# Kernel tuning notes

Hardware: AMD Instinct MI355X
Metric: run time of the kernel (lower is better)

Reference implementation:

```python
import jax, jax.numpy as jnp
import numpy as np

ENTREG = 0.1          # blur passed to geomloss SamplesLoss
P_EXP = 2             # p=2 -> squared euclidean cost
EPS = ENTREG ** P_EXP # geomloss temperature eps = blur**p = 0.01
N_ITERS = 30          # fixed Sinkhorn iterations (geomloss tensorized loop)


def _squared_distances(x, y):
    # C[i,j] = ||x_i - y_j||^2  (geomloss.utils.squared_distances)
    x2 = jnp.sum(x * x, axis=-1)  # [n]
    y2 = jnp.sum(y * y, axis=-1)  # [m]
    return x2[:, None] + y2[None, :] - 2.0 * (x @ y.T)


def setup_inputs() -> dict:
    key = jax.random.key(0)
    k1, k2 = jax.random.split(key)
    Xs = jax.random.normal(k1, (4096, 1024), dtype=jnp.float32)
    Xt = jax.random.normal(k2, (4096, 1024), dtype=jnp.float32)
    return {"Xs": Xs, "Xt": Xt}


def _sinkhorn_plan(Xs, Xt):
    n, m = Xs.shape[0], Xt.shape[0]
    C = _squared_distances(Xs, Xt)          # [n, m]
    loga = -jnp.log(jnp.float32(n))         # uniform source weights (log)
    logb = -jnp.log(jnp.float32(m))         # uniform target weights (log)
    f0 = jnp.zeros((n,), dtype=C.dtype)
    g0 = jnp.zeros((m,), dtype=C.dtype)

    def step(carry, _):
        f, g = carry
        # softmin updates in log-domain (stable logsumexp), eps = blur**p
        g = -EPS * jax.nn.logsumexp((f[:, None] - C) / EPS + loga, axis=0)  # [m]
        f = -EPS * jax.nn.logsumexp((g[None, :] - C) / EPS + logb, axis=1)  # [n]
        return (f, g), None

    (f, g), _ = jax.lax.scan(jax.checkpoint(step), (f0, g0), None, length=N_ITERS)
    # closs: P = exp((u^T + v - C) / entreg)  -- note: entreg, not eps, as in source
    P = jnp.exp((f[:, None] + g[None, :] - C) / ENTREG)
    return P


def reference(Xs, Xt):
    return _sinkhorn_plan(Xs, Xt)
```

## Files before the change

kernel.cpp:

```cpp
#include <hip/hip_runtime.h>
#include <cstddef>
#include <cstdint>

#define N_PTS 4096
#define DIMK 1024

typedef _Float16 half8 __attribute__((ext_vector_type(8)));
typedef float floatx4 __attribute__((ext_vector_type(4)));

static constexpr float S_SCALE = 144.26950408889634f;
static constexpr float TWO_S   = 288.53900817779268f;
static constexpr float NEG_BIG = -3.4e38f;


__global__ __launch_bounds__(256) void k_prep(const float* __restrict__ Xs,
                                              float* __restrict__ fvec) {
  int row  = blockIdx.x * 4 + (threadIdx.x >> 6);
  int lane = threadIdx.x & 63;
  const float* src = Xs + (size_t)row * DIMK;
  float s = 0.f;
#pragma unroll
  for (int r = 0; r < 4; ++r) {
    float4 a = *(const float4*)(src + lane * 4 + r * 256);
    s += a.x * a.x + a.y * a.y + a.z * a.z + a.w * a.w;
  }
#pragma unroll
  for (int off = 32; off; off >>= 1) s += __shfl_xor(s, off);
  if (lane == 0) fvec[row] = (1024.0f - s) * S_SCALE;
}

__global__ __launch_bounds__(256) void k_convert(const float* __restrict__ X,
                                                 _Float16* __restrict__ H,
                                                 _Float16* __restrict__ L) {
  size_t i8 = ((size_t)blockIdx.x * 256 + threadIdx.x) * 8;
  float4 a = *(const float4*)(X + i8);
  float4 b = *(const float4*)(X + i8 + 4);
  float v[8] = {a.x, a.y, a.z, a.w, b.x, b.y, b.z, b.w};
  half8 h, l;
#pragma unroll
  for (int q = 0; q < 8; ++q) {
    _Float16 hh = (_Float16)v[q];
    h[q] = hh;
    l[q] = (_Float16)(v[q] - (float)hh);
  }
  *(half8*)(H + i8) = h;
  *(half8*)(L + i8) = l;
}

__global__ __launch_bounds__(256) void k_gemm_mfma(const _Float16* __restrict__ Ah,
                                                   const _Float16* __restrict__ Al,
                                                   const _Float16* __restrict__ Bh,
                                                   const _Float16* __restrict__ Bl,
                                                   float* __restrict__ D,
                                                   float* __restrict__ DT) {
  __shared__ __align__(16) _Float16 Ahs[128 * 32];
  __shared__ __align__(16) _Float16 Als[128 * 32];
  __shared__ __align__(16) _Float16 Bhs[128 * 32];
  __shared__ __align__(16) _Float16 Bls[128 * 32];
  const int t    = threadIdx.x;
  const int lane = t & 63, wave = t >> 6;
  const int wm = wave >> 1, wn = wave & 1;
  const int lm = lane & 15, q = lane >> 4;
  const int row0 = blockIdx.y * 128, col0 = blockIdx.x * 128;

  floatx4 acc[4][4];
#pragma unroll
  for (int i = 0; i < 4; ++i)
#pragma unroll
    for (int j = 0; j < 4; ++j) acc[i][j] = (floatx4){0.f, 0.f, 0.f, 0.f};

  const int r0 = t >> 2, p0 = t & 3;
  const int r1 = 64 + r0;

  for (int k0 = 0; k0 < DIMK; k0 += 32) {
    size_t ga0 = (size_t)(row0 + r0) * DIMK + k0 + p0 * 8;
    size_t ga1 = (size_t)(row0 + r1) * DIMK + k0 + p0 * 8;
    size_t gb0 = (size_t)(col0 + r0) * DIMK + k0 + p0 * 8;
    size_t gb1 = (size_t)(col0 + r1) * DIMK + k0 + p0 * 8;
    half8 vah0 = *(const half8*)(Ah + ga0);
    half8 vah1 = *(const half8*)(Ah + ga1);
    half8 val0 = *(const half8*)(Al + ga0);
    half8 val1 = *(const half8*)(Al + ga1);
    half8 vbh0 = *(const half8*)(Bh + gb0);
    half8 vbh1 = *(const half8*)(Bh + gb1);
    half8 vbl0 = *(const half8*)(Bl + gb0);
    half8 vbl1 = *(const half8*)(Bl + gb1);
    __syncthreads();
    ((half8*)Ahs)[t] = vah0; ((half8*)Ahs)[t + 256] = vah1;
    ((half8*)Als)[t] = val0; ((half8*)Als)[t + 256] = val1;
    ((half8*)Bhs)[t] = vbh0; ((half8*)Bhs)[t + 256] = vbh1;
    ((half8*)Bls)[t] = vbl0; ((half8*)Bls)[t + 256] = vbl1;
    __syncthreads();

    half8 afh[4], afl[4], bfh[4], bfl[4];
#pragma unroll
    for (int i = 0; i < 4; ++i) {
      int ar = (wm * 64 + i * 16 + lm) * 32 + q * 8;
      int br = (wn * 64 + i * 16 + lm) * 32 + q * 8;
      afh[i] = *(const half8*)(Ahs + ar);
      afl[i] = *(const half8*)(Als + ar);
      bfh[i] = *(const half8*)(Bhs + br);
      bfl[i] = *(const half8*)(Bls + br);
    }
#pragma unroll
    for (int i = 0; i < 4; ++i)
#pragma unroll
      for (int j = 0; j < 4; ++j) {
        acc[i][j] = __builtin_amdgcn_mfma_f32_16x16x32_f16(afh[i], bfh[j], acc[i][j], 0, 0, 0);
        acc[i][j] = __builtin_amdgcn_mfma_f32_16x16x32_f16(afh[i], bfl[j], acc[i][j], 0, 0, 0);
        acc[i][j] = __builtin_amdgcn_mfma_f32_16x16x32_f16(afl[i], bfh[j], acc[i][j], 0, 0, 0);
      }
  }

#pragma unroll
  for (int i = 0; i < 4; ++i) {
    int mbase = row0 + wm * 64 + i * 16 + q * 4;
#pragma unroll
    for (int j = 0; j < 4; ++j) {
      int n = col0 + wn * 64 + j * 16 + lm;
      float vals[4];
#pragma unroll
      for (int r = 0; r < 4; ++r) {
        float vv = -TWO_S * acc[i][j][r];
        vals[r] = vv;
        D[(size_t)(mbase + r) * N_PTS + n] = vv;
      }
      if (DT) *(float4*)(DT + (size_t)n * N_PTS + mbase) = *(float4*)vals;
    }
  }
}

__global__ __launch_bounds__(256) void k_gemm(const float* __restrict__ A,
                                              const float* __restrict__ B,
                                              float* __restrict__ D) {
  __shared__ float As[16][132];
  __shared__ float Bs[16][132];
  const int t  = threadIdx.x;
  const int tx = t & 15, ty = t >> 4;
  const int row0 = blockIdx.y * 128, col0 = blockIdx.x * 128;
  float acc[8][8];
#pragma unroll
  for (int i = 0; i < 8; ++i)
#pragma unroll
    for (int j = 0; j < 8; ++j) acc[i][j] = 0.f;
  for (int k0 = 0; k0 < DIMK; k0 += 16) {
#pragma unroll
    for (int s2 = 0; s2 < 2; ++s2) {
      int f4i = t + s2 * 256;
      int r   = f4i >> 2;
      int kp  = (f4i & 3) << 2;
      float4 a4 = *(const float4*)(A + (size_t)(row0 + r) * DIMK + k0 + kp);
      float4 b4 = *(const float4*)(B + (size_t)(col0 + r) * DIMK + k0 + kp);
      As[kp + 0][r] = a4.x; As[kp + 1][r] = a4.y; As[kp + 2][r] = a4.z; As[kp + 3][r] = a4.w;
      Bs[kp + 0][r] = b4.x; Bs[kp + 1][r] = b4.y; Bs[kp + 2][r] = b4.z; Bs[kp + 3][r] = b4.w;
    }
    __syncthreads();
#pragma unroll
    for (int kk = 0; kk < 16; ++kk) {
      float a[8], b[8];
      *(float4*)(a)     = *(const float4*)(&As[kk][ty * 4]);
      *(float4*)(a + 4) = *(const float4*)(&As[kk][64 + ty * 4]);
      *(float4*)(b)     = *(const float4*)(&Bs[kk][tx * 4]);
      *(float4*)(b + 4) = *(const float4*)(&Bs[kk][64 + tx * 4]);
#pragma unroll
      for (int i = 0; i < 8; ++i)
#pragma unroll
        for (int j = 0; j < 8; ++j) acc[i][j] = fmaf(a[i], b[j], acc[i][j]);
    }
    __syncthreads();
  }
#pragma unroll
  for (int i = 0; i < 8; ++i) {
    int r = row0 + ((i < 4) ? (ty * 4 + i) : (64 + ty * 4 + (i - 4)));
    float* out = D + (size_t)r * N_PTS + col0;
    float4 o1, o2;
    o1.x = -TWO_S * acc[i][0]; o1.y = -TWO_S * acc[i][1];
    o1.z = -TWO_S * acc[i][2]; o1.w = -TWO_S * acc[i][3];
    o2.x = -TWO_S * acc[i][4]; o2.y = -TWO_S * acc[i][5];
    o2.z = -TWO_S * acc[i][6]; o2.w = -TWO_S * acc[i][7];
    *(float4*)(out + tx * 4)      = o1;
    *(float4*)(out + 64 + tx * 4) = o2;
  }
}

__global__ __launch_bounds__(256) void k_sweep(const float* __restrict__ Mrow,
                                               const float* __restrict__ vin,
                                               float* __restrict__ vout) {
  const int t = threadIdx.x;
  const int l = t & 63;
  const int row = blockIdx.x * 4 + (t >> 6);
  const float* rp_ = Mrow + (size_t)row * N_PTS;
  float M = NEG_BIG, S = 0.f;
#pragma unroll
  for (int c = 0; c < 4; ++c) {
    float v[16];
#pragma unroll
    for (int qq = 0; qq < 4; ++qq) {
      int j = l * 4 + (c * 4 + qq) * 256;
      float4 d = *(const float4*)(rp_ + j);
      float4 g = *(const float4*)(vin + j);
      v[qq * 4 + 0] = g.x - d.x;
      v[qq * 4 + 1] = g.y - d.y;
      v[qq * 4 + 2] = g.z - d.z;
      v[qq * 4 + 3] = g.w - d.w;
    }
    float Mc = v[0];
#pragma unroll
    for (int qq = 1; qq < 16; ++qq) Mc = fmaxf(Mc, v[qq]);
    float Mn = fmaxf(M, Mc);
    float s  = S * exp2f(M - Mn);
#pragma unroll
    for (int qq = 0; qq < 16; ++qq) s += exp2f(v[qq] - Mn);
    M = Mn; S = s;
  }
#pragma unroll
  for (int off = 32; off; off >>= 1) {
    float M2 = __shfl_xor(M, off);
    float S2 = __shfl_xor(S, off);
    float Mn = fmaxf(M, M2);
    S = S * exp2f(M - Mn) + S2 * exp2f(M2 - Mn);
    M = Mn;
  }
  if (l == 0) vout[row] = 12.0f - M - log2f(S);
}

__device__ __forceinline__ float4 f4max(float4 a, float4 b) {
  return make_float4(fmaxf(a.x, b.x), fmaxf(a.y, b.y), fmaxf(a.z, b.z), fmaxf(a.w, b.w));
}
__device__ __forceinline__ void msmerge(float4& M, float4& S, const float4 M2, const float4 S2) {
  float4 Mn = f4max(M, M2);
  S.x = S.x * exp2f(M.x - Mn.x) + S2.x * exp2f(M2.x - Mn.x);
  S.y = S.y * exp2f(M.y - Mn.y) + S2.y * exp2f(M2.y - Mn.y);
  S.z = S.z * exp2f(M.z - Mn.z) + S2.z * exp2f(M2.z - Mn.z);
  S.w = S.w * exp2f(M.w - Mn.w) + S2.w * exp2f(M2.w - Mn.w);
  M = Mn;
}
__global__ __launch_bounds__(1024) void k_colpass(const float* __restrict__ D,
                                                  const float* __restrict__ fvec,
                                                  float* __restrict__ gvec) {
  __shared__ float fs[N_PTS];
  __shared__ float4 MS[16][4][2];
  const int t = threadIdx.x;
  *(float4*)(fs + t * 4) = *(const float4*)(fvec + t * 4);
  __syncthreads();
  const int c4 = t & 3;
  const int rp = t >> 2;
  const float* base = D + blockIdx.x * 16 + c4 * 4;
  float4 M = make_float4(NEG_BIG, NEG_BIG, NEG_BIG, NEG_BIG);
  float4 S = make_float4(0.f, 0.f, 0.f, 0.f);
#pragma unroll
  for (int h = 0; h < 2; ++h) {
    float4 v[8];
#pragma unroll
    for (int qq = 0; qq < 8; ++qq) {
      int r = rp + (h * 8 + qq) * 256;
      float4 d = *(const float4*)(base + (size_t)r * N_PTS);
      float fr = fs[r];
      v[qq] = make_float4(fr - d.x, fr - d.y, fr - d.z, fr - d.w);
    }
    float4 Mc = f4max(f4max(f4max(v[0], v[1]), f4max(v[2], v[3])),
                      f4max(f4max(v[4], v[5]), f4max(v[6], v[7])));
    float4 Mn = f4max(M, Mc);
    float4 s;
    s.x = S.x * exp2f(M.x - Mn.x);
    s.y = S.y * exp2f(M.y - Mn.y);
    s.z = S.z * exp2f(M.z - Mn.z);
    s.w = S.w * exp2f(M.w - Mn.w);
#pragma unroll
    for (int qq = 0; qq < 8; ++qq) {
      s.x += exp2f(v[qq].x - Mn.x);
      s.y += exp2f(v[qq].y - Mn.y);
      s.z += exp2f(v[qq].z - Mn.z);
      s.w += exp2f(v[qq].w - Mn.w);
    }
    M = Mn; S = s;
  }
#pragma unroll
  for (int off = 4; off <= 32; off <<= 1) {
    float4 M2, S2;
    M2.x = __shfl_xor(M.x, off); M2.y = __shfl_xor(M.y, off);
    M2.z = __shfl_xor(M.z, off); M2.w = __shfl_xor(M.w, off);
    S2.x = __shfl_xor(S.x, off); S2.y = __shfl_xor(S.y, off);
    S2.z = __shfl_xor(S.z, off); S2.w = __shfl_xor(S.w, off);
    msmerge(M, S, M2, S2);
  }
  const int wv = t >> 6, l = t & 63;
  if (l < 4) { MS[wv][l][0] = M; MS[wv][l][1] = S; }
  __syncthreads();
  if (t < 4) {
    float4 M0 = MS[0][t][0], S0 = MS[0][t][1];
#pragma unroll
    for (int w = 1; w < 16; ++w) msmerge(M0, S0, MS[w][t][0], MS[w][t][1]);
    float4 g;
    g.x = 12.0f - M0.x - log2f(S0.x);
    g.y = 12.0f - M0.y - log2f(S0.y);
    g.z = 12.0f - M0.z - log2f(S0.z);
    g.w = 12.0f - M0.w - log2f(S0.w);
    *(float4*)(gvec + blockIdx.x * 16 + t * 4) = g;
  }
}

__global__ __launch_bounds__(256) void k_final(float* __restrict__ D,
                                               const float* __restrict__ fvec,
                                               const float* __restrict__ gvec) {
  size_t idx = ((size_t)blockIdx.x * 256 + threadIdx.x) * 8;
  int i = (int)(idx >> 12);
  int j = (int)(idx & (N_PTS - 1));
  float fi = fvec[i];
#pragma unroll
  for (int h = 0; h < 2; ++h) {
    float4 d  = *(float4*)(D + idx + h * 4);
    float4 g4 = *(const float4*)(gvec + j + h * 4);
    d.x = exp2f(0.1f * (fi + g4.x - d.x));
    d.y = exp2f(0.1f * (fi + g4.y - d.y));
    d.z = exp2f(0.1f * (fi + g4.z - d.z));
    d.w = exp2f(0.1f * (fi + g4.w - d.w));
    *(float4*)(D + idx + h * 4) = d;
  }
}

extern "C" void kernel_launch(void* const* d_in, const int* in_sizes, int n_in,
                              void* d_out, int out_size, void* d_ws, size_t ws_size,
                              hipStream_t stream) {
  const float* Xs = (const float*)d_in[0];
  const float* Xt = (const float*)d_in[1];
  float* D   = (float*)d_out;
  char* wsb  = (char*)d_ws;
  float* fvec = (float*)wsb;
  float* gvec = fvec + N_PTS;

  const size_t halfElems  = (size_t)N_PTS * DIMK;
  const size_t offHalves  = 32768;
  _Float16* Ah = (_Float16*)(wsb + offHalves);
  _Float16* Al = Ah + halfElems;
  _Float16* Bh = Al + halfElems;
  _Float16* Bl = Bh + halfElems;
  float* DT    = (float*)(wsb + offHalves + 4 * halfElems * sizeof(_Float16));
  const size_t needHalves = offHalves + 4 * halfElems * sizeof(_Float16);
  const size_t needFull   = needHalves + (size_t)N_PTS * N_PTS * sizeof(float);
  const bool haveH = ws_size >= needHalves;
  const bool haveT = ws_size >= needFull;

  k_prep<<<1024, 256, 0, stream>>>(Xs, fvec);
  if (haveH) {
    k_convert<<<2048, 256, 0, stream>>>(Xs, Ah, Al);
    k_convert<<<2048, 256, 0, stream>>>(Xt, Bh, Bl);
    k_gemm_mfma<<<dim3(32, 32), 256, 0, stream>>>(Ah, Al, Bh, Bl, D, haveT ? DT : nullptr);
  } else {
    k_gemm<<<dim3(32, 32), 256, 0, stream>>>(Xs, Xt, D);
  }
  for (int it = 0; it < 30; ++it) {
    if (haveT) k_sweep<<<1024, 256, 0, stream>>>(DT, fvec, gvec);
    else       k_colpass<<<256, 1024, 0, stream>>>(D, fvec, gvec);
    k_sweep<<<1024, 256, 0, stream>>>(D, gvec, fvec);
  }
  k_final<<<8192, 256, 0, stream>>>(D, fvec, gvec);
}
```

Measured before the change: 964.6 us.

## Replace transposed cost matrix with split column logsumexp over row-major matrix

Stops writing a transposed copy of the 64MB cost matrix in the GEMM epilogue. The column softmin is now read straight from the row-major matrix by a two-stage reduction: 32 row-chunk partial max/sum pairs per column, then a small merge kernel. This removes 64MB of GEMM writes and the large workspace, but adds one extra launch per iteration and partial buffers. Column reads are coalesced float4 loads across rows.

```diff
diff --git a/kernel.cpp b/kernel.cpp
--- a/kernel.cpp
+++ b/kernel.cpp
@@ -12,6 +12,18 @@
 static constexpr float TWO_S   = 288.53900817779268f;
 static constexpr float NEG_BIG = -3.4e38f;
 
+
+__device__ __forceinline__ float4 f4max(float4 a, float4 b) {
+  return make_float4(fmaxf(a.x, b.x), fmaxf(a.y, b.y), fmaxf(a.z, b.z), fmaxf(a.w, b.w));
+}
+__device__ __forceinline__ void msmerge(float4& M, float4& S, const float4 M2, const float4 S2) {
+  float4 Mn = f4max(M, M2);
+  S.x = S.x * exp2f(M.x - Mn.x) + S2.x * exp2f(M2.x - Mn.x);
+  S.y = S.y * exp2f(M.y - Mn.y) + S2.y * exp2f(M2.y - Mn.y);
+  S.z = S.z * exp2f(M.z - Mn.z) + S2.z * exp2f(M2.z - Mn.z);
+  S.w = S.w * exp2f(M.w - Mn.w) + S2.w * exp2f(M2.w - Mn.w);
+  M = Mn;
+}
 
 __global__ __launch_bounds__(256) void k_prep(const float* __restrict__ Xs,
                                               float* __restrict__ fvec) {
@@ -51,8 +63,7 @@
                                                    const _Float16* __restrict__ Al,
                                                    const _Float16* __restrict__ Bh,
                                                    const _Float16* __restrict__ Bl,
-                                                   float* __restrict__ D,
-                                                   float* __restrict__ DT) {
+                                                   float* __restrict__ D) {
   __shared__ __align__(16) _Float16 Ahs[128 * 32];
   __shared__ __align__(16) _Float16 Als[128 * 32];
   __shared__ __align__(16) _Float16 Bhs[128 * 32];
@@ -118,14 +129,9 @@
 #pragma unroll
     for (int j = 0; j < 4; ++j) {
       int n = col0 + wn * 64 + j * 16 + lm;
-      float vals[4];
-#pragma unroll
-      for (int r = 0; r < 4; ++r) {
-        float vv = -TWO_S * acc[i][j][r];
-        vals[r] = vv;
-        D[(size_t)(mbase + r) * N_PTS + n] = vv;
-      }
-      if (DT) *(float4*)(DT + (size_t)n * N_PTS + mbase) = *(float4*)vals;
+#pragma unroll
+      for (int r = 0; r < 4; ++r)
+        D[(size_t)(mbase + r) * N_PTS + n] = -TWO_S * acc[i][j][r];
     }
   }
 }
@@ -183,6 +189,69 @@
   }
 }
 
+__global__ __launch_bounds__(256) void k_colpassT(const float* __restrict__ D,
+                                                  const float* __restrict__ fvec,
+                                                  float* __restrict__ PM,
+                                                  float* __restrict__ PS) {
+  const int t = threadIdx.x;
+  const int l = t & 63, w = t >> 6;
+  const int c0 = blockIdx.x * 256 + l * 4;
+  const int r0 = blockIdx.y * 128;
+  float4 M = make_float4(NEG_BIG, NEG_BIG, NEG_BIG, NEG_BIG);
+  float4 S = make_float4(0.f, 0.f, 0.f, 0.f);
+#pragma unroll
+  for (int c = 0; c < 4; ++c) {
+    float4 v[8];
+#pragma unroll
+    for (int q = 0; q < 8; ++q) {
+      int row = r0 + (c * 8 + q) * 4 + w;
+      float fr = fvec[row];
+      float4 d = *(const float4*)(D + (size_t)row * N_PTS + c0);
+      v[q] = make_float4(fr - d.x, fr - d.y, fr - d.z, fr - d.w);
+    }
+    float4 Mc = f4max(f4max(f4max(v[0], v[1]), f4max(v[2], v[3])),
+                      f4max(f4max(v[4], v[5]), f4max(v[6], v[7])));
+    float4 Mn = f4max(M, Mc);
+    float4 s;
+    s.x = S.x * exp2f(M.x - Mn.x);
+    s.y = S.y * exp2f(M.y - Mn.y);
+    s.z = S.z * exp2f(M.z - Mn.z);
+    s.w = S.w * exp2f(M.w - Mn.w);
+#pragma unroll
+    for (int q = 0; q < 8; ++q) {
+      s.x += exp2f(v[q].x - Mn.x);
+      s.y += exp2f(v[q].y - Mn.y);
+      s.z += exp2f(v[q].z - Mn.z);
+      s.w += exp2f(v[q].w - Mn.w);
+    }
+    M = Mn; S = s;
+  }
+  __shared__ float4 LM[4][64], LS[4][64];
+  LM[w][l] = M; LS[w][l] = S;
+  __syncthreads();
+  if (w == 0) {
+#pragma unroll
+    for (int p = 1; p < 4; ++p) msmerge(M, S, LM[p][l], LS[p][l]);
+    *(float4*)(PM + (size_t)blockIdx.y * N_PTS + c0) = M;
+    *(float4*)(PS + (size_t)blockIdx.y * N_PTS + c0) = S;
+  }
+}
+
+__global__ __launch_bounds__(256) void k_colmerge(const float* __restrict__ PM,
+                                                  const float* __restrict__ PS,
+                                                  float* __restrict__ gvec) {
+  int c = blockIdx.x * 256 + threadIdx.x;
+  float M = PM[c], S = PS[c];
+#pragma unroll 8
+  for (int p = 1; p < 32; ++p) {
+    float M1 = PM[(size_t)p * N_PTS + c], S1 = PS[(size_t)p * N_PTS + c];
+    float Mn = fmaxf(M, M1);
+    S = S * exp2f(M - Mn) + S1 * exp2f(M1 - Mn);
+    M = Mn;
+  }
+  gvec[c] = 12.0f - M - log2f(S);
+}
+
 __global__ __launch_bounds__(256) void k_sweep(const float* __restrict__ Mrow,
                                                const float* __restrict__ vin,
                                                float* __restrict__ vout) {
@@ -224,17 +293,6 @@
   if (l == 0) vout[row] = 12.0f - M - log2f(S);
 }
 
-__device__ __forceinline__ float4 f4max(float4 a, float4 b) {
-  return make_float4(fmaxf(a.x, b.x), fmaxf(a.y, b.y), fmaxf(a.z, b.z), fmaxf(a.w, b.w));
-}
-__device__ __forceinline__ void msmerge(float4& M, float4& S, const float4 M2, const float4 S2) {
-  float4 Mn = f4max(M, M2);
-  S.x = S.x * exp2f(M.x - Mn.x) + S2.x * exp2f(M2.x - Mn.x);
-  S.y = S.y * exp2f(M.y - Mn.y) + S2.y * exp2f(M2.y - Mn.y);
-  S.z = S.z * exp2f(M.z - Mn.z) + S2.z * exp2f(M2.z - Mn.z);
-  S.w = S.w * exp2f(M.w - Mn.w) + S2.w * exp2f(M2.w - Mn.w);
-  M = Mn;
-}
 __global__ __launch_bounds__(1024) void k_colpass(const float* __restrict__ D,
                                                   const float* __restrict__ fvec,
                                                   float* __restrict__ gvec) {
@@ -329,15 +387,16 @@
   float* fvec = (float*)wsb;
   float* gvec = fvec + N_PTS;
 
-  const size_t halfElems  = (size_t)N_PTS * DIMK;
-  const size_t offHalves  = 32768;
+  const size_t halfElems = (size_t)N_PTS * DIMK;
+  const size_t offHalves = 32768;
   _Float16* Ah = (_Float16*)(wsb + offHalves);
   _Float16* Al = Ah + halfElems;
   _Float16* Bh = Al + halfElems;
   _Float16* Bl = Bh + halfElems;
-  float* DT    = (float*)(wsb + offHalves + 4 * halfElems * sizeof(_Float16));
+  float* PM = (float*)(wsb + offHalves + 4 * halfElems * sizeof(_Float16));
+  float* PS = PM + 32 * N_PTS;
   const size_t needHalves = offHalves + 4 * halfElems * sizeof(_Float16);
-  const size_t needFull   = needHalves + (size_t)N_PTS * N_PTS * sizeof(float);
+  const size_t needFull   = needHalves + 2 * 32 * N_PTS * sizeof(float);
   const bool haveH = ws_size >= needHalves;
   const bool haveT = ws_size >= needFull;
 
@@ -345,13 +404,17 @@
   if (haveH) {
     k_convert<<<2048, 256, 0, stream>>>(Xs, Ah, Al);
     k_convert<<<2048, 256, 0, stream>>>(Xt, Bh, Bl);
-    k_gemm_mfma<<<dim3(32, 32), 256, 0, stream>>>(Ah, Al, Bh, Bl, D, haveT ? DT : nullptr);
+    k_gemm_mfma<<<dim3(32, 32), 256, 0, stream>>>(Ah, Al, Bh, Bl, D);
   } else {
     k_gemm<<<dim3(32, 32), 256, 0, stream>>>(Xs, Xt, D);
   }
   for (int it = 0; it < 30; ++it) {
-    if (haveT) k_sweep<<<1024, 256, 0, stream>>>(DT, fvec, gvec);
-    else       k_colpass<<<256, 1024, 0, stream>>>(D, fvec, gvec);
+    if (haveT) {
+      k_colpassT<<<dim3(16, 32), 256, 0, stream>>>(D, fvec, PM, PS);
+      k_colmerge<<<16, 256, 0, stream>>>(PM, PS, gvec);
+    } else {
+      k_colpass<<<256, 1024, 0, stream>>>(D, fvec, gvec);
+    }
     k_sweep<<<1024, 256, 0, stream>>>(D, gvec, fvec);
   }
   k_final<<<8192, 256, 0, stream>>>(D, fvec, gvec);
```

After: 1.328 ms. 1.38x slower.

## Fuse Sinkhorn iterations and final exp into one cooperative persistent kernel

Applied to the files above, without the earlier changes.

Replaces the 60 per-iteration sweep launches plus the final kernel with a single cooperative kernel of 256 blocks x 512 threads. The kernel alternates column and row logsumexp passes separated by grid.sync and then writes the transport plan in place. Each wave now preloads a whole 4096-float row into registers before reducing, to expose more memory-level parallelism. The aim is to remove launch overhead and inter-kernel gaps, at the cost of grid-wide barrier latency, a fixed grid that may under-occupy the GPU, and higher register pressure.

```diff
diff --git a/kernel.cpp b/kernel.cpp
--- a/kernel.cpp
+++ b/kernel.cpp
@@ -1,6 +1,9 @@
 #include <hip/hip_runtime.h>
+#include <hip/hip_cooperative_groups.h>
 #include <cstddef>
 #include <cstdint>
+
+namespace cg = cooperative_groups;
 
 #define N_PTS 4096
 #define DIMK 1024
@@ -12,6 +15,18 @@
 static constexpr float TWO_S   = 288.53900817779268f;
 static constexpr float NEG_BIG = -3.4e38f;
 
+
+__device__ __forceinline__ float4 f4max(float4 a, float4 b) {
+  return make_float4(fmaxf(a.x, b.x), fmaxf(a.y, b.y), fmaxf(a.z, b.z), fmaxf(a.w, b.w));
+}
+__device__ __forceinline__ void msmerge(float4& M, float4& S, const float4 M2, const float4 S2) {
+  float4 Mn = f4max(M, M2);
+  S.x = S.x * exp2f(M.x - Mn.x) + S2.x * exp2f(M2.x - Mn.x);
+  S.y = S.y * exp2f(M.y - Mn.y) + S2.y * exp2f(M2.y - Mn.y);
+  S.z = S.z * exp2f(M.z - Mn.z) + S2.z * exp2f(M2.z - Mn.z);
+  S.w = S.w * exp2f(M.w - Mn.w) + S2.w * exp2f(M2.w - Mn.w);
+  M = Mn;
+}
 
 __global__ __launch_bounds__(256) void k_prep(const float* __restrict__ Xs,
                                               float* __restrict__ fvec) {
@@ -183,34 +198,31 @@
   }
 }
 
-__global__ __launch_bounds__(256) void k_sweep(const float* __restrict__ Mrow,
-                                               const float* __restrict__ vin,
-                                               float* __restrict__ vout) {
-  const int t = threadIdx.x;
-  const int l = t & 63;
-  const int row = blockIdx.x * 4 + (t >> 6);
-  const float* rp_ = Mrow + (size_t)row * N_PTS;
+__device__ __forceinline__ float lse_row4096(const float* __restrict__ rowp,
+                                             const float* __restrict__ vin,
+                                             int l) {
+  float4 dv[16], gv[16];
+#pragma unroll
+  for (int k = 0; k < 16; ++k) dv[k] = *(const float4*)(rowp + l * 4 + k * 256);
+#pragma unroll
+  for (int k = 0; k < 16; ++k) gv[k] = *(const float4*)(vin + l * 4 + k * 256);
   float M = NEG_BIG, S = 0.f;
 #pragma unroll
   for (int c = 0; c < 4; ++c) {
     float v[16];
 #pragma unroll
-    for (int qq = 0; qq < 4; ++qq) {
-      int j = l * 4 + (c * 4 + qq) * 256;
-      float4 d = *(const float4*)(rp_ + j);
-      float4 g = *(const float4*)(vin + j);
-      v[qq * 4 + 0] = g.x - d.x;
-      v[qq * 4 + 1] = g.y - d.y;
-      v[qq * 4 + 2] = g.z - d.z;
-      v[qq * 4 + 3] = g.w - d.w;
+    for (int q = 0; q < 4; ++q) {
+      float4 d = dv[c * 4 + q], g = gv[c * 4 + q];
+      v[q * 4 + 0] = g.x - d.x; v[q * 4 + 1] = g.y - d.y;
+      v[q * 4 + 2] = g.z - d.z; v[q * 4 + 3] = g.w - d.w;
     }
     float Mc = v[0];
 #pragma unroll
-    for (int qq = 1; qq < 16; ++qq) Mc = fmaxf(Mc, v[qq]);
+    for (int q = 1; q < 16; ++q) Mc = fmaxf(Mc, v[q]);
     float Mn = fmaxf(M, Mc);
-    float s  = S * exp2f(M - Mn);
-#pragma unroll
-    for (int qq = 0; qq < 16; ++qq) s += exp2f(v[qq] - Mn);
+    float s = S * exp2f(M - Mn);
+#pragma unroll
+    for (int q = 0; q < 16; ++q) s += exp2f(v[q] - Mn);
     M = Mn; S = s;
   }
 #pragma unroll
@@ -221,20 +233,62 @@
     S = S * exp2f(M - Mn) + S2 * exp2f(M2 - Mn);
     M = Mn;
   }
-  if (l == 0) vout[row] = 12.0f - M - log2f(S);
-}
-
-__device__ __forceinline__ float4 f4max(float4 a, float4 b) {
-  return make_float4(fmaxf(a.x, b.x), fmaxf(a.y, b.y), fmaxf(a.z, b.z), fmaxf(a.w, b.w));
-}
-__device__ __forceinline__ void msmerge(float4& M, float4& S, const float4 M2, const float4 S2) {
-  float4 Mn = f4max(M, M2);
-  S.x = S.x * exp2f(M.x - Mn.x) + S2.x * exp2f(M2.x - Mn.x);
-  S.y = S.y * exp2f(M.y - Mn.y) + S2.y * exp2f(M2.y - Mn.y);
-  S.z = S.z * exp2f(M.z - Mn.z) + S2.z * exp2f(M2.z - Mn.z);
-  S.w = S.w * exp2f(M.w - Mn.w) + S2.w * exp2f(M2.w - Mn.w);
-  M = Mn;
-}
+  return 12.0f - M - log2f(S);
+}
+
+__global__ __launch_bounds__(512, 2) void k_loop(float* __restrict__ D,
+                                                 const float* __restrict__ DT,
+                                                 float* __restrict__ fvec,
+                                                 float* __restrict__ gvec) {
+  cg::grid_group grid = cg::this_grid();
+  const int t = threadIdx.x;
+  const int l = t & 63, w = t >> 6;
+  const int base = blockIdx.x * 16 + w * 2;
+
+  for (int it = 0; it < 30; ++it) {
+#pragma unroll
+    for (int h = 0; h < 2; ++h) {
+      int c = base + h;
+      float g = lse_row4096(DT + (size_t)c * N_PTS, fvec, l);
+      if (l == 0) gvec[c] = g;
+    }
+    grid.sync();
+#pragma unroll
+    for (int h = 0; h < 2; ++h) {
+      int r = base + h;
+      float f = lse_row4096(D + (size_t)r * N_PTS, gvec, l);
+      if (l == 0) fvec[r] = f;
+    }
+    grid.sync();
+  }
+#pragma unroll
+  for (int h = 0; h < 2; ++h) {
+    int r = base + h;
+    float fi = fvec[r];
+    float* rp = D + (size_t)r * N_PTS;
+#pragma unroll 4
+    for (int k = 0; k < 16; ++k) {
+      int j = l * 4 + k * 256;
+      float4 d  = *(const float4*)(rp + j);
+      float4 g4 = *(const float4*)(gvec + j);
+      d.x = exp2f(0.1f * (fi + g4.x - d.x));
+      d.y = exp2f(0.1f * (fi + g4.y - d.y));
+      d.z = exp2f(0.1f * (fi + g4.z - d.z));
+      d.w = exp2f(0.1f * (fi + g4.w - d.w));
+      *(float4*)(rp + j) = d;
+    }
+  }
+}
+
+__global__ __launch_bounds__(256) void k_sweep(const float* __restrict__ Mrow,
+                                               const float* __restrict__ vin,
+                                               float* __restrict__ vout) {
+  const int l = threadIdx.x & 63;
+  const int row = blockIdx.x * 4 + (threadIdx.x >> 6);
+  float r = lse_row4096(Mrow + (size_t)row * N_PTS, vin, l);
+  if (l == 0) vout[row] = r;
+}
+
 __global__ __launch_bounds__(1024) void k_colpass(const float* __restrict__ D,
                                                   const float* __restrict__ fvec,
                                                   float* __restrict__ gvec) {
@@ -329,13 +383,13 @@
   float* fvec = (float*)wsb;
   float* gvec = fvec + N_PTS;
 
-  const size_t halfElems  = (size_t)N_PTS * DIMK;
-  const size_t offHalves  = 32768;
+  const size_t halfElems = (size_t)N_PTS * DIMK;
+  const size_t offHalves = 32768;
   _Float16* Ah = (_Float16*)(wsb + offHalves);
   _Float16* Al = Ah + halfElems;
   _Float16* Bh = Al + halfElems;
   _Float16* Bl = Bh + halfElems;
-  float* DT    = (float*)(wsb + offHalves + 4 * halfElems * sizeof(_Float16));
+  float* DT = (float*)(wsb + offHalves + 4 * halfElems * sizeof(_Float16));
   const size_t needHalves = offHalves + 4 * halfElems * sizeof(_Float16);
   const size_t needFull   = needHalves + (size_t)N_PTS * N_PTS * sizeof(float);
   const bool haveH = ws_size >= needHalves;
@@ -349,10 +403,15 @@
   } else {
     k_gemm<<<dim3(32, 32), 256, 0, stream>>>(Xs, Xt, D);
   }
-  for (int it = 0; it < 30; ++it) {
-    if (haveT) k_sweep<<<1024, 256, 0, stream>>>(DT, fvec, gvec);
-    else       k_colpass<<<256, 1024, 0, stream>>>(D, fvec, gvec);
-    k_sweep<<<1024, 256, 0, stream>>>(D, gvec, fvec);
-  }
-  k_final<<<8192, 256, 0, stream>>>(D, fvec, gvec);
-}
+
+  if (haveT) {
+    void* args[] = {(void*)&D, (void*)&DT, (void*)&fvec, (void*)&gvec};
+    hipLaunchCooperativeKernel((const void*)k_loop, dim3(256), dim3(512), args, 0, stream);
+  } else {
+    for (int it = 0; it < 30; ++it) {
+      k_colpass<<<256, 1024, 0, stream>>>(D, fvec, gvec);
+      k_sweep<<<1024, 256, 0, stream>>>(D, gvec, fvec);
+    }
+    k_final<<<8192, 256, 0, stream>>>(D, fvec, gvec);
+  }
+}
```

Result: slower. 2.889 ms (+199.5%).
